# Kernel optimization log

Measured on AMD Instinct MI355X. Metric: run time of the kernel, lower is better.

## Reference

```python
import jax, jax.numpy as jnp
import numpy as np
import math

B, S, E = 1, 1024, 2880          # batch, seq, hidden_size
H, KV, D = 64, 8, 64             # query heads, kv heads, head_dim
WIN = 128                        # sliding window
BASE, SCALE, ORIG = 150000.0, 32.0, 4096
BFAST, BSLOW = 32.0, 1.0
SCALING = D ** -0.5
NEG = jnp.finfo(jnp.float32).min


def _rope_tables(positions):
    """YaRN-scaled RoPE cos/sin tables, matching RotaryEmbedding._build_cache."""
    def find_dim(rot):
        return D * math.log(ORIG / (rot * 2 * math.pi)) / (2 * math.log(BASE))
    low = max(find_dim(BFAST), 0.0)
    high = min(find_dim(BSLOW), D // 2 - 1)
    if low == high:
        high += 0.001
    pos_freqs = BASE ** (jnp.arange(0, D, 2, dtype=jnp.float32) / D)
    ramp = jnp.clip((jnp.arange(D // 2, dtype=jnp.float32) - low) / (high - low), 0.0, 1.0)
    inv_freq = (1.0 / (SCALE * pos_freqs)) * ramp + (1.0 / pos_freqs) * (1.0 - ramp)
    mscale = 0.1 * math.log(SCALE) + 1.0
    ang = positions.astype(jnp.float32)[:, None] * inv_freq[None, :]   # [S, D/2]
    emb = jnp.concatenate([ang, ang], axis=-1)                          # [S, D]
    return jnp.cos(emb) * mscale, jnp.sin(emb) * mscale


def _apply_rope(x, cos, sin):
    # x: [B, S, h, D]; cos/sin: [S, D]
    c = cos[None, :, None, :]
    s = sin[None, :, None, :]
    half = D // 2
    rot = jnp.concatenate([-x[..., half:], x[..., :half]], axis=-1)
    return x * c + rot * s


def setup_inputs() -> dict:
    key = jax.random.key(0)
    ks = jax.random.split(key, 10)
    std = 0.02
    return {
        "hidden_states": jax.random.normal(ks[0], (B, S, E), jnp.float32),
        "positions": jnp.arange(S, dtype=jnp.int32),
        "Wq": jax.random.normal(ks[1], (H * D, E), jnp.float32) * std,
        "bq": jax.random.normal(ks[2], (H * D,), jnp.float32) * std,
        "Wk": jax.random.normal(ks[3], (KV * D, E), jnp.float32) * std,
        "bk": jax.random.normal(ks[4], (KV * D,), jnp.float32) * std,
        "Wv": jax.random.normal(ks[5], (KV * D, E), jnp.float32) * std,
        "bv": jax.random.normal(ks[6], (KV * D,), jnp.float32) * std,
        "Wo": jax.random.normal(ks[7], (E, H * D), jnp.float32) * std,
        "bo": jax.random.normal(ks[8], (E,), jnp.float32) * std,
        "sinks": jax.random.normal(ks[9], (H,), jnp.float32) * 0.5,
    }


def reference(hidden_states, positions, Wq, bq, Wk, bk, Wv, bv, Wo, bo, sinks):
    x = hidden_states
    q = (x @ Wq.T + bq).reshape(B, S, H, D)
    k = (x @ Wk.T + bk).reshape(B, S, KV, D)
    v = (x @ Wv.T + bv).reshape(B, S, KV, D)

    cos, sin = _rope_tables(positions)
    q = _apply_rope(q, cos, sin)
    k = _apply_rope(k, cos, sin)

    rep = H // KV  # GQA: each kv head serves 8 query heads
    k = jnp.repeat(k, rep, axis=2)  # [B, S, H, D]
    v = jnp.repeat(v, rep, axis=2)

    scores = jnp.einsum("bqhd,bkhd->bhqk", q, k) * SCALING  # [B, H, S, S]
    i = jnp.arange(S)
    allowed = (i[None, :] <= i[:, None]) & (i[:, None] - i[None, :] < WIN)  # causal + window
    scores = jnp.where(allowed[None, None], scores, NEG)

    # learned per-head sink logit joins the softmax denominator
    sink = jnp.broadcast_to(sinks[None, :, None, None], (B, H, S, 1))
    probs = jax.nn.softmax(jnp.concatenate([scores, sink], axis=-1), axis=-1)[..., :-1]

    out = jnp.einsum("bhqk,bkhd->bqhd", probs, v).reshape(B, S, H * D)
    return out @ Wo.T + bo
```

## Files before the change

### kernel.cpp

```cpp
#include <hip/hip_runtime.h>
#include <math.h>

#define S_LEN 1024
#define QKV_N 5120

typedef __attribute__((ext_vector_type(8))) __bf16 bf16x8;
typedef __attribute__((ext_vector_type(4))) float f32x4;

__device__ __forceinline__ unsigned short f2bf(float f) {
  unsigned int u = __float_as_uint(f);
  u += 0x7fff + ((u >> 16) & 1);
  return (unsigned short)(u >> 16);
}
__device__ __forceinline__ float bf2f(unsigned short u) {
  return __uint_as_float((unsigned int)u << 16);
}

__device__ __forceinline__ void async_copy16(const void* g, void* l) {
  __builtin_amdgcn_global_load_lds(
      (const __attribute__((address_space(1))) unsigned int*)g,
      (__attribute__((address_space(3))) unsigned int*)l, 16, 0, 0);
}

__global__ void cvt_bf16(const float* __restrict__ in, unsigned short* __restrict__ out, int n4) {
  int i = blockIdx.x * 256 + threadIdx.x;
  if (i >= n4) return;
  float4 v = ((const float4*)in)[i];
  ushort4 r;
  r.x = f2bf(v.x); r.y = f2bf(v.y); r.z = f2bf(v.z); r.w = f2bf(v.w);
  ((ushort4*)out)[i] = r;
}

__global__ void concat_bias(const float* __restrict__ bq, const float* __restrict__ bk,
                            const float* __restrict__ bv, float* __restrict__ o) {
  int i = blockIdx.x * 256 + threadIdx.x;
  if (i >= 5120) return;
  o[i] = (i < 4096) ? bq[i] : ((i < 4608) ? bk[i - 4096] : bv[i - 4608]);
}

__global__ void rope_tables(const int* __restrict__ positions, float* __restrict__ cosT,
                            float* __restrict__ sinT, float low, float high, float mscale) {
  int idx = blockIdx.x * 256 + threadIdx.x;
  if (idx >= S_LEN * 32) return;
  int j = idx & 31, s = idx >> 5;
  float pf = powf(150000.0f, (float)j / 32.0f);
  float ramp = ((float)j - low) / (high - low);
  ramp = fminf(fmaxf(ramp, 0.0f), 1.0f);
  float invf = (1.0f / (32.0f * pf)) * ramp + (1.0f / pf) * (1.0f - ramp);
  float ang = (float)positions[s] * invf;
  cosT[idx] = cosf(ang) * mscale;
  sinT[idx] = sinf(ang) * mscale;
}

__global__ void rope_kernel(const unsigned short* __restrict__ qkvb,
                            const float* __restrict__ cosT, const float* __restrict__ sinT,
                            unsigned short* __restrict__ Qb, unsigned short* __restrict__ Kb) {
  int idx = blockIdx.x * 256 + threadIdx.x;
  if (idx >= S_LEN * 72 * 32) return;
  int j = idx & 31;
  int hh = (idx >> 5) % 72;
  int s = idx / (72 * 32);
  const unsigned short* base = qkvb + (size_t)s * QKV_N + hh * 64;
  float x = bf2f(base[j]), y = bf2f(base[j + 32]);
  float c = cosT[s * 32 + j], sn = sinT[s * 32 + j];
  float o1 = x * c - y * sn;
  float o2 = y * c + x * sn;
  if (hh < 64) {
    unsigned short* q = Qb + ((size_t)s * 64 + hh) * 64;
    q[j]      = f2bf(o1 * 0.125f);
    q[j + 32] = f2bf(o2 * 0.125f);
  } else {
    unsigned short* k = Kb + ((size_t)s * 8 + (hh - 64)) * 64;
    k[j]      = f2bf(o1);
    k[j + 32] = f2bf(o2);
  }
}

__global__ __launch_bounds__(256) void v_transpose(const unsigned short* __restrict__ qkvb,
                                                   unsigned short* __restrict__ Vt) {
  __shared__ unsigned short tile[128][66];
  const int kvh = blockIdx.x, s0 = blockIdx.y * 128;
  const int t = threadIdx.x;
#pragma unroll
  for (int i = 0; i < 32; i++) {
    int e = t + i * 256;
    int s = e >> 6, d = e & 63;
    tile[s][d] = qkvb[(size_t)(s0 + s) * QKV_N + 4608 + kvh * 64 + d];
  }
  __syncthreads();
#pragma unroll
  for (int i = 0; i < 32; i++) {
    int e = t + i * 256;
    int d = e >> 7, s = e & 127;
    Vt[((size_t)kvh * 64 + d) * 1024 + s0 + s] = tile[s][d];
  }
}

template <bool BF16_OUT>
__global__ __launch_bounds__(256) void gemm_bt(
    const unsigned short* __restrict__ A, const unsigned short* __restrict__ B,
    const float* __restrict__ bias, void* __restrict__ Cv, int M, int N, int K) {
  __shared__ __align__(16) unsigned short As[128 * 32];
  __shared__ __align__(16) unsigned short Bs[128 * 32];
  const int t = threadIdx.x;
  const int l = t & 63;
  const int w = t >> 6;
  const int lr = l & 15, lq = l >> 4;
  const int m0 = blockIdx.y * 128, n0 = blockIdx.x * 128;
  const int wm = (w >> 1) * 64, wn = (w & 1) * 64;

  const int rowA = t >> 2;
  const int kg = (t & 3) * 8;

  int rb0 = n0 + rowA;      if (rb0 > N - 1) rb0 = N - 1;
  int rb1 = n0 + rowA + 64; if (rb1 > N - 1) rb1 = N - 1;

  const unsigned short* gA0 = A + (size_t)(m0 + rowA) * K + kg;
  const unsigned short* gA1 = gA0 + (size_t)64 * K;
  const unsigned short* gB0 = B + (size_t)rb0 * K + kg;
  const unsigned short* gB1 = B + (size_t)rb1 * K + kg;

  unsigned short* lA0 = &As[t * 8];
  unsigned short* lA1 = &As[(t + 256) * 8];
  unsigned short* lB0 = &Bs[t * 8];
  unsigned short* lB1 = &Bs[(t + 256) * 8];

  f32x4 acc[4][4] = {};

  for (int k0 = 0; k0 < K; k0 += 32) {
    async_copy16(gA0 + k0, lA0);
    async_copy16(gA1 + k0, lA1);
    async_copy16(gB0 + k0, lB0);
    async_copy16(gB1 + k0, lB1);
    __syncthreads();
    bf16x8 af[4], bf[4];
#pragma unroll
    for (int i = 0; i < 4; i++)
      af[i] = *(const bf16x8*)&As[(wm + i * 16 + lr) * 32 + lq * 8];
#pragma unroll
    for (int i = 0; i < 4; i++)
      bf[i] = *(const bf16x8*)&Bs[(wn + i * 16 + lr) * 32 + lq * 8];
#pragma unroll
    for (int mi = 0; mi < 4; mi++)
#pragma unroll
      for (int ni = 0; ni < 4; ni++)
        acc[mi][ni] = __builtin_amdgcn_mfma_f32_16x16x32_bf16(af[mi], bf[ni], acc[mi][ni], 0, 0, 0);
    __syncthreads();
  }

#pragma unroll
  for (int mi = 0; mi < 4; mi++) {
#pragma unroll
    for (int ni = 0; ni < 4; ni++) {
      int col = n0 + wn + ni * 16 + lr;
      if (col < N) {
        float bv = bias[col];
#pragma unroll
        for (int r = 0; r < 4; r++) {
          int row = m0 + wm + mi * 16 + lq * 4 + r;
          float val = acc[mi][ni][r] + bv;
          if (BF16_OUT)
            ((unsigned short*)Cv)[(size_t)row * N + col] = f2bf(val);
          else
            ((float*)Cv)[(size_t)row * N + col] = val;
        }
      }
    }
  }
}

__global__ __launch_bounds__(64) void attn_mfma(
    const unsigned short* __restrict__ Qb,
    const unsigned short* __restrict__ Kb,
    const unsigned short* __restrict__ Vt,
    const float* __restrict__ sinks,
    unsigned short* __restrict__ out) {
  const int h = blockIdx.x;
  const int q0 = blockIdx.y * 16;
  const int kvh = h >> 3;
  const int l = threadIdx.x;
  const int n = l & 15;
  const int g = l >> 4;

  __shared__ __align__(16) unsigned short Pl[16][32];

  const unsigned short* qp = Qb + (((size_t)(q0 + n) * 64 + h) * 64 + g * 8);
  bf16x8 qf0 = *(const bf16x8*)qp;
  bf16x8 qf1 = *(const bf16x8*)(qp + 32);

  const int q_lane = q0 + n;
  int k_lo = q0 - 127; if (k_lo < 0) k_lo = 0;
  k_lo &= ~31;
  const int k_end = q0 + 16;

  float m = -3.0e38f, lsum = 0.0f;
  f32x4 oacc[4] = {};

  for (int kk = k_lo; kk < k_end; kk += 32) {
    int kr0 = kk + n;      if (kr0 > 1023) kr0 = 1023;
    int kr1 = kk + 16 + n; if (kr1 > 1023) kr1 = 1023;
    const unsigned short* kp0 = Kb + (((size_t)kr0 * 8 + kvh) * 64 + g * 8);
    const unsigned short* kp1 = Kb + (((size_t)kr1 * 8 + kvh) * 64 + g * 8);
    bf16x8 ka0 = *(const bf16x8*)kp0;
    bf16x8 ka1 = *(const bf16x8*)(kp0 + 32);
    bf16x8 kb0 = *(const bf16x8*)kp1;
    bf16x8 kb1 = *(const bf16x8*)(kp1 + 32);
    f32x4 st0 = {}, st1 = {};
    st0 = __builtin_amdgcn_mfma_f32_16x16x32_bf16(ka0, qf0, st0, 0, 0, 0);
    st0 = __builtin_amdgcn_mfma_f32_16x16x32_bf16(ka1, qf1, st0, 0, 0, 0);
    st1 = __builtin_amdgcn_mfma_f32_16x16x32_bf16(kb0, qf0, st1, 0, 0, 0);
    st1 = __builtin_amdgcn_mfma_f32_16x16x32_bf16(kb1, qf1, st1, 0, 0, 0);

    float tm = -3.0e38f;
#pragma unroll
    for (int r = 0; r < 4; r++) {
      int k0i = kk + 4 * g + r;
      int k1i = k0i + 16;
      bool ok0 = (k0i <= q_lane) && (q_lane - k0i < 128);
      bool ok1 = (k1i <= q_lane) && (q_lane - k1i < 128);
      st0[r] = ok0 ? st0[r] : -3.0e38f;
      st1[r] = ok1 ? st1[r] : -3.0e38f;
      tm = fmaxf(tm, fmaxf(st0[r], st1[r]));
    }
    tm = fmaxf(tm, __shfl_xor(tm, 16));
    tm = fmaxf(tm, __shfl_xor(tm, 32));

    float mn = fmaxf(m, tm);
    float corr = __expf(m - mn);
    m = mn;
    float p0[4], p1[4], ps = 0.0f;
#pragma unroll
    for (int r = 0; r < 4; r++) {
      p0[r] = __expf(st0[r] - mn);
      p1[r] = __expf(st1[r] - mn);
      ps += p0[r] + p1[r];
    }
    ps += __shfl_xor(ps, 16);
    ps += __shfl_xor(ps, 32);
    lsum = lsum * corr + ps;

    ushort4 w0, w1;
    w0.x = f2bf(p0[0]); w0.y = f2bf(p0[1]); w0.z = f2bf(p0[2]); w0.w = f2bf(p0[3]);
    w1.x = f2bf(p1[0]); w1.y = f2bf(p1[1]); w1.z = f2bf(p1[2]); w1.w = f2bf(p1[3]);
    *(ushort4*)&Pl[n][4 * g]      = w0;
    *(ushort4*)&Pl[n][16 + 4 * g] = w1;
    __syncthreads();
    bf16x8 pf = *(const bf16x8*)&Pl[n][8 * g];
    __syncthreads();

#pragma unroll
    for (int db = 0; db < 4; db++) {
      const unsigned short* vp = Vt + ((size_t)(kvh * 64 + db * 16 + n)) * 1024 + kk + 8 * g;
      bf16x8 vf = *(const bf16x8*)vp;
#pragma unroll
      for (int r = 0; r < 4; r++) oacc[db][r] *= corr;
      oacc[db] = __builtin_amdgcn_mfma_f32_16x16x32_bf16(vf, pf, oacc[db], 0, 0, 0);
    }
  }

  float sink = sinks[h];
  float mn2 = fmaxf(m, sink);
  float corr2 = __expf(m - mn2);
  float denom = lsum * corr2 + __expf(sink - mn2);
  float fs = corr2 / denom;

#pragma unroll
  for (int db = 0; db < 4; db++) {
    ushort4 r;
    r.x = f2bf(oacc[db][0] * fs);
    r.y = f2bf(oacc[db][1] * fs);
    r.z = f2bf(oacc[db][2] * fs);
    r.w = f2bf(oacc[db][3] * fs);
    *(ushort4*)(out + (size_t)q_lane * 4096 + h * 64 + db * 16 + 4 * g) = r;
  }
}

extern "C" void kernel_launch(void* const* d_in, const int* in_sizes, int n_in,
                              void* d_out, int out_size, void* d_ws, size_t ws_size,
                              hipStream_t stream) {
  const float* x = (const float*)d_in[0];
  const int* positions = (const int*)d_in[1];
  const float* Wq = (const float*)d_in[2];
  const float* bq = (const float*)d_in[3];
  const float* Wk = (const float*)d_in[4];
  const float* bk = (const float*)d_in[5];
  const float* Wv = (const float*)d_in[6];
  const float* bv = (const float*)d_in[7];
  const float* Wo = (const float*)d_in[8];
  const float* bo = (const float*)d_in[9];
  const float* sinks = (const float*)d_in[10];
  float* out = (float*)d_out;

  char* ws = (char*)d_ws;
  unsigned short* xb    = (unsigned short*)(ws + 0);
  unsigned short* wqkv  = (unsigned short*)(ws + 5898240);
  unsigned short* wo    = (unsigned short*)(ws + 35389440);
  float* bqkv           = (float*)(ws + 58982400);
  unsigned short* qkvb  = (unsigned short*)(ws + 59002880);
  unsigned short* attnb = (unsigned short*)(ws + 69488640);
  unsigned short* Qb    = (unsigned short*)(ws + 77877248);
  unsigned short* Kb    = (unsigned short*)(ws + 86265856);
  unsigned short* Vt    = (unsigned short*)(ws + 87314432);
  float* cosT           = (float*)(ws + 88367104);
  float* sinT           = (float*)(ws + 88498176);

  cvt_bf16<<<2880, 256, 0, stream>>>(x, xb, 737280);
  cvt_bf16<<<11520, 256, 0, stream>>>(Wq, wqkv, 2949120);
  cvt_bf16<<<1440, 256, 0, stream>>>(Wk, wqkv + (size_t)4096 * 2880, 368640);
  cvt_bf16<<<1440, 256, 0, stream>>>(Wv, wqkv + (size_t)4608 * 2880, 368640);
  cvt_bf16<<<11520, 256, 0, stream>>>(Wo, wo, 2949120);
  concat_bias<<<20, 256, 0, stream>>>(bq, bk, bv, bqkv);

  const double TWO_PI = 6.283185307179586;
  double lowd = 64.0 * log(4096.0 / (32.0 * TWO_PI)) / (2.0 * log(150000.0));
  if (lowd < 0.0) lowd = 0.0;
  double highd = 64.0 * log(4096.0 / (1.0 * TWO_PI)) / (2.0 * log(150000.0));
  if (highd > 31.0) highd = 31.0;
  if (lowd == highd) highd += 0.001;
  float mscale = (float)(0.1 * log(32.0) + 1.0);
  rope_tables<<<128, 256, 0, stream>>>(positions, cosT, sinT, (float)lowd, (float)highd, mscale);

  gemm_bt<true><<<dim3(40, 8), 256, 0, stream>>>(xb, wqkv, bqkv, qkvb, 1024, 5120, 2880);
  rope_kernel<<<9216, 256, 0, stream>>>(qkvb, cosT, sinT, Qb, Kb);
  v_transpose<<<dim3(8, 8), 256, 0, stream>>>(qkvb, Vt);
  attn_mfma<<<dim3(64, 64), 64, 0, stream>>>(Qb, Kb, Vt, sinks, attnb);
  gemm_bt<false><<<dim3(23, 8), 256, 0, stream>>>(attnb, wo, bo, out, 1024, 2880, 4096);
}
```

Baseline: 373.4 us.

## Split-K both projection GEMMs with partial buffers and separate reduce kernels

Replaces the single-pass GEMM with a split-K variant that writes fp32 partial tiles per K slice, followed by reduction kernels that sum the partials, add bias and convert to bf16 or fp32. The aim is to fill more of the device's compute units, since the original grids (320 and 184 blocks) are small relative to the CU count. The grid is also reordered so M varies fastest. In exchange it adds extra global traffic for the partial buffers (up to 80MB written and read for QKV) plus two extra launches, and the split factor depends on the workspace size.

Result: faster. 338.9 us (-9.2%).

```diff
diff --git a/kernel.cpp b/kernel.cpp
--- a/kernel.cpp
+++ b/kernel.cpp
@@ -96,18 +96,22 @@
   }
 }
 
-template <bool BF16_OUT>
-__global__ __launch_bounds__(256) void gemm_bt(
+__global__ __launch_bounds__(256) void gemm_bt_sk(
     const unsigned short* __restrict__ A, const unsigned short* __restrict__ B,
-    const float* __restrict__ bias, void* __restrict__ Cv, int M, int N, int K) {
+    float* __restrict__ part, int M, int N, int K) {
   __shared__ __align__(16) unsigned short As[128 * 32];
   __shared__ __align__(16) unsigned short Bs[128 * 32];
   const int t = threadIdx.x;
   const int l = t & 63;
   const int w = t >> 6;
   const int lr = l & 15, lq = l >> 4;
-  const int m0 = blockIdx.y * 128, n0 = blockIdx.x * 128;
+  const int m0 = blockIdx.x * 128, n0 = blockIdx.y * 128;
+  const int s = blockIdx.z, SP = gridDim.z;
   const int wm = (w >> 1) * 64, wn = (w & 1) * 64;
+
+  const int T = K >> 5;
+  const int kb = ((s * T) / SP) * 32;
+  const int ke = (((s + 1) * T) / SP) * 32;
 
   const int rowA = t >> 2;
   const int kg = (t & 3) * 8;
@@ -127,7 +131,7 @@
 
   f32x4 acc[4][4] = {};
 
-  for (int k0 = 0; k0 < K; k0 += 32) {
+  for (int k0 = kb; k0 < ke; k0 += 32) {
     async_copy16(gA0 + k0, lA0);
     async_copy16(gA1 + k0, lA1);
     async_copy16(gB0 + k0, lB0);
@@ -148,25 +152,51 @@
     __syncthreads();
   }
 
+  float* P = part + (size_t)s * M * N;
 #pragma unroll
   for (int mi = 0; mi < 4; mi++) {
 #pragma unroll
     for (int ni = 0; ni < 4; ni++) {
       int col = n0 + wn + ni * 16 + lr;
       if (col < N) {
-        float bv = bias[col];
 #pragma unroll
         for (int r = 0; r < 4; r++) {
           int row = m0 + wm + mi * 16 + lq * 4 + r;
-          float val = acc[mi][ni][r] + bv;
-          if (BF16_OUT)
-            ((unsigned short*)Cv)[(size_t)row * N + col] = f2bf(val);
-          else
-            ((float*)Cv)[(size_t)row * N + col] = val;
+          P[(size_t)row * N + col] = acc[mi][ni][r];
         }
       }
     }
   }
+}
+
+__global__ void reduce_bf16(const float* __restrict__ part, const float* __restrict__ bias,
+                            unsigned short* __restrict__ out, int n4, int ncols4, int SP) {
+  int i = blockIdx.x * 256 + threadIdx.x;
+  if (i >= n4) return;
+  float4 a = ((const float4*)part)[i];
+  for (int s = 1; s < SP; s++) {
+    float4 b = ((const float4*)part)[(size_t)s * n4 + i];
+    a.x += b.x; a.y += b.y; a.z += b.z; a.w += b.w;
+  }
+  float4 bv = ((const float4*)bias)[i % ncols4];
+  ushort4 r;
+  r.x = f2bf(a.x + bv.x); r.y = f2bf(a.y + bv.y);
+  r.z = f2bf(a.z + bv.z); r.w = f2bf(a.w + bv.w);
+  ((ushort4*)out)[i] = r;
+}
+
+__global__ void reduce_f32(const float* __restrict__ part, const float* __restrict__ bias,
+                           float* __restrict__ out, int n4, int ncols4, int SP) {
+  int i = blockIdx.x * 256 + threadIdx.x;
+  if (i >= n4) return;
+  float4 a = ((const float4*)part)[i];
+  for (int s = 1; s < SP; s++) {
+    float4 b = ((const float4*)part)[(size_t)s * n4 + i];
+    a.x += b.x; a.y += b.y; a.z += b.z; a.w += b.w;
+  }
+  float4 bv = ((const float4*)bias)[i % ncols4];
+  a.x += bv.x; a.y += bv.y; a.z += bv.z; a.w += bv.w;
+  ((float4*)out)[i] = a;
 }
 
 __global__ __launch_bounds__(64) void attn_mfma(
@@ -297,12 +327,21 @@
   unsigned short* wo    = (unsigned short*)(ws + 35389440);
   float* bqkv           = (float*)(ws + 58982400);
   unsigned short* qkvb  = (unsigned short*)(ws + 59002880);
-  unsigned short* attnb = (unsigned short*)(ws + 69488640);
-  unsigned short* Qb    = (unsigned short*)(ws + 77877248);
-  unsigned short* Kb    = (unsigned short*)(ws + 86265856);
-  unsigned short* Vt    = (unsigned short*)(ws + 87314432);
-  float* cosT           = (float*)(ws + 88367104);
-  float* sinT           = (float*)(ws + 88498176);
+  float* cosT           = (float*)(ws + 69488640);
+  float* sinT           = (float*)(ws + 69619712);
+  const size_t R = 69750784;
+  float* qkv_part       = (float*)(ws + R);
+  unsigned short* Qb    = (unsigned short*)(ws + R);
+  unsigned short* Kb    = (unsigned short*)(ws + R + 8388608);
+  unsigned short* Vt    = (unsigned short*)(ws + R + 9437184);
+  unsigned short* attnb = (unsigned short*)(ws + R + 10489856);
+  float* out_part       = (float*)(ws + R + 18878464);
+
+  int split_q = 1, split_o = 1;
+  if (ws_size >= R + 4ull * 20971520) split_q = 4;
+  else if (ws_size >= R + 2ull * 20971520) split_q = 2;
+  if (ws_size >= R + 18878464 + 4ull * 11796480) split_o = 4;
+  else if (ws_size >= R + 18878464 + 2ull * 11796480) split_o = 2;
 
   cvt_bf16<<<2880, 256, 0, stream>>>(x, xb, 737280);
   cvt_bf16<<<11520, 256, 0, stream>>>(Wq, wqkv, 2949120);
@@ -320,9 +359,13 @@
   float mscale = (float)(0.1 * log(32.0) + 1.0);
   rope_tables<<<128, 256, 0, stream>>>(positions, cosT, sinT, (float)lowd, (float)highd, mscale);
 
-  gemm_bt<true><<<dim3(40, 8), 256, 0, stream>>>(xb, wqkv, bqkv, qkvb, 1024, 5120, 2880);
+  gemm_bt_sk<<<dim3(8, 40, split_q), 256, 0, stream>>>(xb, wqkv, qkv_part, 1024, 5120, 2880);
+  reduce_bf16<<<5120, 256, 0, stream>>>(qkv_part, bqkv, qkvb, 1310720, 1280, split_q);
+
   rope_kernel<<<9216, 256, 0, stream>>>(qkvb, cosT, sinT, Qb, Kb);
   v_transpose<<<dim3(8, 8), 256, 0, stream>>>(qkvb, Vt);
   attn_mfma<<<dim3(64, 64), 64, 0, stream>>>(Qb, Kb, Vt, sinks, attnb);
-  gemm_bt<false><<<dim3(23, 8), 256, 0, stream>>>(attnb, wo, bo, out, 1024, 2880, 4096);
-}
+
+  gemm_bt_sk<<<dim3(8, 23, split_o), 256, 0, stream>>>(attnb, wo, out_part, 1024, 2880, 4096);
+  reduce_f32<<<2880, 256, 0, stream>>>(out_part, bo, out, 737280, 720, split_o);
+}
```

## Split-K both projection GEMMs with bf16 partials and fused reduction

Applied to the files above, without the earlier changes.

Both the QKV and output projection GEMMs now split the K dimension into 4 slices (2 if the workspace is small), each writing a bf16 partial tile. Tiles are ordered so that blocks sharing A rows are adjacent. The intent is more blocks than the 320 or 184 the GEMMs had, so all CUs stay busy. The partial sums are added back in the rope and V-transpose kernels for QKV, and in a new vectorized reduce kernel for the output. The cost is extra partial-buffer traffic and bf16 rounding of each partial, which loses some precision before bias is added.

Measured after the change: 335.1 us. 10.2% less time.

```diff
diff --git a/kernel.cpp b/kernel.cpp
--- a/kernel.cpp
+++ b/kernel.cpp
@@ -52,16 +52,21 @@
   sinT[idx] = sinf(ang) * mscale;
 }
 
-__global__ void rope_kernel(const unsigned short* __restrict__ qkvb,
-                            const float* __restrict__ cosT, const float* __restrict__ sinT,
-                            unsigned short* __restrict__ Qb, unsigned short* __restrict__ Kb) {
+__global__ void rope_qk(const unsigned short* __restrict__ part, const float* __restrict__ bqkv,
+                        const float* __restrict__ cosT, const float* __restrict__ sinT,
+                        unsigned short* __restrict__ Qb, unsigned short* __restrict__ Kb, int SP) {
   int idx = blockIdx.x * 256 + threadIdx.x;
   if (idx >= S_LEN * 72 * 32) return;
   int j = idx & 31;
   int hh = (idx >> 5) % 72;
   int s = idx / (72 * 32);
-  const unsigned short* base = qkvb + (size_t)s * QKV_N + hh * 64;
-  float x = bf2f(base[j]), y = bf2f(base[j + 32]);
+  int c1 = hh * 64 + j, c2 = c1 + 32;
+  float x = bqkv[c1], y = bqkv[c2];
+  for (int sp = 0; sp < SP; sp++) {
+    const unsigned short* P = part + (size_t)sp * S_LEN * QKV_N + (size_t)s * QKV_N;
+    x += bf2f(P[c1]);
+    y += bf2f(P[c2]);
+  }
   float c = cosT[s * 32 + j], sn = sinT[s * 32 + j];
   float o1 = x * c - y * sn;
   float o2 = y * c + x * sn;
@@ -76,8 +81,9 @@
   }
 }
 
-__global__ __launch_bounds__(256) void v_transpose(const unsigned short* __restrict__ qkvb,
-                                                   unsigned short* __restrict__ Vt) {
+__global__ __launch_bounds__(256) void v_trans(const unsigned short* __restrict__ part,
+                                               const float* __restrict__ bqkv,
+                                               unsigned short* __restrict__ Vt, int SP) {
   __shared__ unsigned short tile[128][66];
   const int kvh = blockIdx.x, s0 = blockIdx.y * 128;
   const int t = threadIdx.x;
@@ -85,7 +91,11 @@
   for (int i = 0; i < 32; i++) {
     int e = t + i * 256;
     int s = e >> 6, d = e & 63;
-    tile[s][d] = qkvb[(size_t)(s0 + s) * QKV_N + 4608 + kvh * 64 + d];
+    int col = 4608 + kvh * 64 + d;
+    float v = bqkv[col];
+    for (int sp = 0; sp < SP; sp++)
+      v += bf2f(part[(size_t)sp * S_LEN * QKV_N + (size_t)(s0 + s) * QKV_N + col]);
+    tile[s][d] = f2bf(v);
   }
   __syncthreads();
 #pragma unroll
@@ -96,18 +106,30 @@
   }
 }
 
-template <bool BF16_OUT>
-__global__ __launch_bounds__(256) void gemm_bt(
+__global__ __launch_bounds__(256) void gemm_bt_sk(
     const unsigned short* __restrict__ A, const unsigned short* __restrict__ B,
-    const float* __restrict__ bias, void* __restrict__ Cv, int M, int N, int K) {
+    unsigned short* __restrict__ part, int M, int N, int K, int NT, int SP) {
   __shared__ __align__(16) unsigned short As[128 * 32];
   __shared__ __align__(16) unsigned short Bs[128 * 32];
+  const int lb = blockIdx.x;
+  const int aI = lb >> 6;
+  const int rem = lb & 63;
+  const int mI = rem >> 3;
+  const int bI = rem & 7;
+  const int c = aI * 8 + bI;
+  if (c >= NT * SP) return;
+  const int sI = c / NT, nI = c % NT;
+  const int m0 = mI * 128, n0 = nI * 128;
+
   const int t = threadIdx.x;
   const int l = t & 63;
   const int w = t >> 6;
   const int lr = l & 15, lq = l >> 4;
-  const int m0 = blockIdx.y * 128, n0 = blockIdx.x * 128;
   const int wm = (w >> 1) * 64, wn = (w & 1) * 64;
+
+  const int T = K >> 5;
+  const int kb = ((sI * T) / SP) * 32;
+  const int ke = (((sI + 1) * T) / SP) * 32;
 
   const int rowA = t >> 2;
   const int kg = (t & 3) * 8;
@@ -127,7 +149,7 @@
 
   f32x4 acc[4][4] = {};
 
-  for (int k0 = 0; k0 < K; k0 += 32) {
+  for (int k0 = kb; k0 < ke; k0 += 32) {
     async_copy16(gA0 + k0, lA0);
     async_copy16(gA1 + k0, lA1);
     async_copy16(gB0 + k0, lB0);
@@ -148,25 +170,41 @@
     __syncthreads();
   }
 
+  unsigned short* P = part + (size_t)sI * M * N;
 #pragma unroll
   for (int mi = 0; mi < 4; mi++) {
 #pragma unroll
     for (int ni = 0; ni < 4; ni++) {
       int col = n0 + wn + ni * 16 + lr;
       if (col < N) {
-        float bv = bias[col];
 #pragma unroll
         for (int r = 0; r < 4; r++) {
           int row = m0 + wm + mi * 16 + lq * 4 + r;
-          float val = acc[mi][ni][r] + bv;
-          if (BF16_OUT)
-            ((unsigned short*)Cv)[(size_t)row * N + col] = f2bf(val);
-          else
-            ((float*)Cv)[(size_t)row * N + col] = val;
+          P[(size_t)row * N + col] = f2bf(acc[mi][ni][r]);
         }
       }
     }
   }
+}
+
+__global__ void reduce_f32(const unsigned short* __restrict__ part, const float* __restrict__ bias,
+                           float* __restrict__ out, int SP) {
+  int i = blockIdx.x * 256 + threadIdx.x;
+  if (i >= 368640) return;
+  float acc[8];
+  int bc = (i % 360) * 8;
+#pragma unroll
+  for (int e = 0; e < 8; e++) acc[e] = bias[bc + e];
+  for (int sp = 0; sp < SP; sp++) {
+    const ushort4* P = (const ushort4*)(part + (size_t)sp * 2949120);
+    ushort4 u0 = P[i * 2], u1 = P[i * 2 + 1];
+    acc[0] += bf2f(u0.x); acc[1] += bf2f(u0.y); acc[2] += bf2f(u0.z); acc[3] += bf2f(u0.w);
+    acc[4] += bf2f(u1.x); acc[5] += bf2f(u1.y); acc[6] += bf2f(u1.z); acc[7] += bf2f(u1.w);
+  }
+  float4 o0 = {acc[0], acc[1], acc[2], acc[3]};
+  float4 o1 = {acc[4], acc[5], acc[6], acc[7]};
+  ((float4*)out)[i * 2] = o0;
+  ((float4*)out)[i * 2 + 1] = o1;
 }
 
 __global__ __launch_bounds__(64) void attn_mfma(
@@ -292,17 +330,29 @@
   float* out = (float*)d_out;
 
   char* ws = (char*)d_ws;
-  unsigned short* xb    = (unsigned short*)(ws + 0);
-  unsigned short* wqkv  = (unsigned short*)(ws + 5898240);
-  unsigned short* wo    = (unsigned short*)(ws + 35389440);
-  float* bqkv           = (float*)(ws + 58982400);
-  unsigned short* qkvb  = (unsigned short*)(ws + 59002880);
-  unsigned short* attnb = (unsigned short*)(ws + 69488640);
-  unsigned short* Qb    = (unsigned short*)(ws + 77877248);
-  unsigned short* Kb    = (unsigned short*)(ws + 86265856);
-  unsigned short* Vt    = (unsigned short*)(ws + 87314432);
-  float* cosT           = (float*)(ws + 88367104);
-  float* sinT           = (float*)(ws + 88498176);
+  unsigned short* xb   = (unsigned short*)(ws + 0);
+  unsigned short* wqkv = (unsigned short*)(ws + 5898240);
+  unsigned short* wo   = (unsigned short*)(ws + 35389440);
+  float* bqkv          = (float*)(ws + 58982400);
+  float* cosT          = (float*)(ws + 59002880);
+  float* sinT          = (float*)(ws + 59133952);
+  const size_t SH = 59265024;
+  unsigned short* qkv_part = (unsigned short*)(ws + SH);
+  unsigned short* out_part = (unsigned short*)(ws + SH);
+  unsigned short* attnb    = (unsigned short*)(ws + SH + 23592960);
+  const size_t TL = SH + 41943040;
+  unsigned short* Qb = (unsigned short*)(ws + TL);
+  unsigned short* Kb = (unsigned short*)(ws + TL + 8388608);
+  unsigned short* Vt = (unsigned short*)(ws + TL + 9437184);
+
+  int split_q = 4, split_o = 4;
+  if (ws_size < TL + 10485888) {
+    split_q = 2; split_o = 2;
+    attnb = (unsigned short*)(ws + SH + 11796480);
+    Qb = (unsigned short*)(ws + SH + 20971520);
+    Kb = Qb + 4194304;
+    Vt = Kb + 524288;
+  }
 
   cvt_bf16<<<2880, 256, 0, stream>>>(x, xb, 737280);
   cvt_bf16<<<11520, 256, 0, stream>>>(Wq, wqkv, 2949120);
@@ -320,9 +370,20 @@
   float mscale = (float)(0.1 * log(32.0) + 1.0);
   rope_tables<<<128, 256, 0, stream>>>(positions, cosT, sinT, (float)lowd, (float)highd, mscale);
 
-  gemm_bt<true><<<dim3(40, 8), 256, 0, stream>>>(xb, wqkv, bqkv, qkvb, 1024, 5120, 2880);
-  rope_kernel<<<9216, 256, 0, stream>>>(qkvb, cosT, sinT, Qb, Kb);
-  v_transpose<<<dim3(8, 8), 256, 0, stream>>>(qkvb, Vt);
+  {
+    int NT = 40, C = NT * split_q;
+    int grid = 64 * ((C + 7) / 8);
+    gemm_bt_sk<<<grid, 256, 0, stream>>>(xb, wqkv, qkv_part, 1024, 5120, 2880, NT, split_q);
+  }
+  rope_qk<<<9216, 256, 0, stream>>>(qkv_part, bqkv, cosT, sinT, Qb, Kb, split_q);
+  v_trans<<<dim3(8, 8), 256, 0, stream>>>(qkv_part, bqkv, Vt, split_q);
+
   attn_mfma<<<dim3(64, 64), 64, 0, stream>>>(Qb, Kb, Vt, sinks, attnb);
-  gemm_bt<false><<<dim3(23, 8), 256, 0, stream>>>(attnb, wo, bo, out, 1024, 2880, 4096);
-}
+
+  {
+    int NT = 23, C = NT * split_o;
+    int grid = 64 * ((C + 7) / 8);
+    gemm_bt_sk<<<grid, 256, 0, stream>>>(attnb, wo, out_part, 1024, 2880, 4096, NT, split_o);
+  }
+  reduce_f32<<<1440, 256, 0, stream>>>(out_part, bo, out, split_o);
+}
```
